# Optimization experiments

Measured on AMD Instinct MI355X. Metric: run time of the kernel, lower is better.

Reference implementation:

```python
import jax, jax.numpy as jnp
import numpy as np

B, S, D, H = 4, 4096, 1024, 8
HD = D // H  # head dims, FFT length for circular convolution


def setup_inputs() -> dict:
    key = jax.random.key(0)
    k1, k2, k3 = jax.random.split(key, 3)
    x = jax.random.normal(k1, (B, S, D), dtype=jnp.float32)
    # torch nn.Linear(D, 3D, bias=False) -> store as [D, 3D] for x @ W
    w_qkv = jax.random.normal(k2, (D, 3 * D), dtype=jnp.float32) * (1.0 / np.sqrt(D))
    w_out = jax.random.normal(k3, (D, D), dtype=jnp.float32) * (1.0 / np.sqrt(D))
    return {"x": x, "w_qkv": w_qkv, "w_out": w_out}


def reference(x, w_qkv, w_out):
    # HRR self-attention (causal, norm=False, dropout in eval mode => identity).
    b, s, d = x.shape
    qkv = x @ w_qkv                               # [B,S,3D]
    q, k, v = jnp.split(qkv, 3, axis=-1)
    q = q.reshape(b, s, H, HD)
    k = k.reshape(b, s, H, HD)
    v = v.reshape(b, s, H, HD)
    # Holographic binding: circular convolution k (*) v == ifft(fft(k)*fft(v))
    fq = jnp.fft.fft(q, axis=-1)                  # [B,S,H,HD] complex
    fk = jnp.fft.fft(k, axis=-1)
    fv = jnp.fft.fft(v, axis=-1)
    kv = fk * fv                                  # bound key-value pairs (freq domain)
    kv = jnp.cumsum(kv, axis=1)                   # causal aggregation over sequence
    # Unbinding via circular correlation with the query: ifft(S * conj(fft(q)))
    vals = jnp.fft.ifft(kv * jnp.conj(fq), axis=-1).real.astype(x.dtype)
    vals = vals.reshape(b, s, d)
    return vals @ w_out
```

## Files before the change

### kernel.cpp

```cpp
#include <hip/hip_runtime.h>

static constexpr int BB = 4;
static constexpr int SS = 4096;
static constexpr int DD = 1024;
static constexpr int HH = 8;
static constexpr int HD = 128;
static constexpr int CS = 32;
static constexpr int NCHUNK = SS / CS;
static constexpr int MROWS = BB * SS;

typedef __attribute__((ext_vector_type(8))) short bfrag;
typedef __attribute__((ext_vector_type(4))) float floatx4;

__device__ __forceinline__ float bf2f(unsigned int u) {
    return __uint_as_float((u & 0xFFFFu) << 16);
}
__device__ __forceinline__ unsigned short f2bf(float f) {
    unsigned int x = __float_as_uint(f);
    unsigned int r = x + 0x7FFFu + ((x >> 16) & 1u);
    return (unsigned short)(r >> 16);
}
__device__ __forceinline__ unsigned int pack_rne(float a, float b) {
    return ((unsigned int)f2bf(a)) | (((unsigned int)f2bf(b)) << 16);
}

__device__ __forceinline__ void async_copy16(const void* g, void* l) {
    __builtin_amdgcn_global_load_lds(
        (const __attribute__((address_space(1))) unsigned int*)g,
        (__attribute__((address_space(3))) unsigned int*)l, 16, 0, 0);
}

struct cpx { float re, im; };

__device__ __forceinline__ cpx cadd(cpx a, cpx b) { return {a.re + b.re, a.im + b.im}; }
__device__ __forceinline__ cpx csub(cpx a, cpx b) { return {a.re - b.re, a.im - b.im}; }
__device__ __forceinline__ cpx cmul(cpx a, cpx b) {
    return { fmaf(a.re, b.re, -a.im * b.im), fmaf(a.re, b.im, a.im * b.re) };
}
__device__ __forceinline__ cpx cmul_cj(cpx a, cpx b) {
    return { fmaf(a.re, b.re, a.im * b.im), fmaf(a.im, b.re, -a.re * b.im) };
}
__device__ __forceinline__ cpx shflx(cpx x, int m) {
    return { __shfl_xor(x.re, m), __shfl_xor(x.im, m) };
}
__device__ __forceinline__ cpx shfl_at(cpx x, int src) {
    return { __shfl(x.re, src), __shfl(x.im, src) };
}

__device__ __forceinline__ int pair_lane_even(int l) {
    int m = (int)(__brev((unsigned)l) >> 26);
    int mp = (64 - m) & 63;
    return (int)(__brev((unsigned)mp) >> 26);
}

__device__ __forceinline__ void make_tw(int lane, cpx tw[7]) {
    const float NEG2PI = -6.28318530717958647692f;
    float a0 = NEG2PI * (float)lane * (1.0f / 128.0f);
    tw[0] = { __cosf(a0), __sinf(a0) };
    int d = 32;
#pragma unroll
    for (int s = 1; s <= 6; ++s) {
        int i = lane & (d - 1);
        float a = NEG2PI * (float)i / (float)(2 * d);
        tw[s] = { __cosf(a), __sinf(a) };
        d >>= 1;
    }
}

__device__ __forceinline__ void fft128_fwd(cpx& x0, cpx& x1, const cpx tw[7], int lane) {
    cpx a = x0, b = x1;
    x0 = cadd(a, b);
    x1 = cmul(csub(a, b), tw[0]);
    int d = 32;
#pragma unroll
    for (int s = 1; s <= 6; ++s) {
        const bool up = (lane & d) != 0;
        cpx o0 = shflx(x0, d);
        cpx o1 = shflx(x1, d);
        cpx s0 = cadd(x0, o0);
        cpx s1 = cadd(x1, o1);
        cpx d0 = cmul(csub(o0, x0), tw[s]);
        cpx d1 = cmul(csub(o1, x1), tw[s]);
        x0 = up ? d0 : s0;
        x1 = up ? d1 : s1;
        d >>= 1;
    }
}

__device__ __forceinline__ void fft128_inv(cpx& x0, cpx& x1, const cpx tw[7], int lane) {
    int d = 1;
#pragma unroll
    for (int s = 6; s >= 1; --s) {
        const bool up = (lane & d) != 0;
        cpx o0 = shflx(x0, d);
        cpx o1 = shflx(x1, d);
        cpx b0 = up ? x0 : o0;
        cpx a0 = up ? o0 : x0;
        cpx b1 = up ? x1 : o1;
        cpx a1 = up ? o1 : x1;
        cpx t0 = cmul_cj(b0, tw[s]);
        cpx t1 = cmul_cj(b1, tw[s]);
        x0 = up ? csub(a0, t0) : cadd(a0, t0);
        x1 = up ? csub(a1, t1) : cadd(a1, t1);
        d <<= 1;
    }
    cpx t = cmul_cj(x1, tw[0]);
    cpx a = x0;
    const float inv = 0.0078125f;
    x0 = { (a.re + t.re) * inv, (a.im + t.im) * inv };
    x1 = { (a.re - t.re) * inv, (a.im - t.im) * inv };
}

__global__ __launch_bounds__(256) void convert_bf16(const float* __restrict__ X,
                                                    unsigned short* __restrict__ Y)
{
    const size_t i = ((size_t)blockIdx.x * 256 + threadIdx.x) * 8;
    float4 v0 = *reinterpret_cast<const float4*>(X + i);
    float4 v1 = *reinterpret_cast<const float4*>(X + i + 4);
    uint4 p = { pack_rne(v0.x, v0.y), pack_rne(v0.z, v0.w),
                pack_rne(v1.x, v1.y), pack_rne(v1.z, v1.w) };
    *reinterpret_cast<uint4*>(Y + i) = p;
}

__global__ __launch_bounds__(256) void transpose_rn(const float* __restrict__ W,
                                                    unsigned short* __restrict__ T,
                                                    int K, int N)
{
    __shared__ float tile[32][33];
    const int n0 = blockIdx.x * 32, k0 = blockIdx.y * 32;
    const int r = threadIdx.x >> 5, c = threadIdx.x & 31;
#pragma unroll
    for (int i = 0; i < 4; ++i)
        tile[r + 8 * i][c] = W[(size_t)(k0 + r + 8 * i) * N + n0 + c];
    __syncthreads();
#pragma unroll
    for (int i = 0; i < 4; ++i) {
        float v = tile[c][r + 8 * i];
        T[(size_t)(n0 + r + 8 * i) * K + k0 + c] = f2bf(v);
    }
}

template <typename OutT>
__global__ __launch_bounds__(256) void gemm_bt(const unsigned short* __restrict__ A,
                                               const unsigned short* __restrict__ Bt,
                                               OutT* __restrict__ C,
                                               int M, int N, int K)
{
    __shared__ __align__(16) unsigned short As[128 * 32];
    __shared__ __align__(16) unsigned short Bs[128 * 32];
    const int tid = threadIdx.x, lane = tid & 63, w = tid >> 6;
    const int wr = w >> 1, wc = w & 1;
    const int m0 = blockIdx.y * 128, n0 = blockIdx.x * 128;

    floatx4 acc[4][4];
#pragma unroll
    for (int i = 0; i < 4; ++i)
#pragma unroll
        for (int j = 0; j < 4; ++j) { floatx4 z = {0.f, 0.f, 0.f, 0.f}; acc[i][j] = z; }

    for (int kt = 0; kt < K; kt += 32) {
#pragma unroll
        for (int i = 0; i < 2; ++i) {
            const int is = 2 * w + i;
            const size_t aoff = (size_t)(m0 + 16 * is + (lane >> 2)) * K + kt + (lane & 3) * 8;
            const size_t boff = (size_t)(n0 + 16 * is + (lane >> 2)) * K + kt + (lane & 3) * 8;
            async_copy16(A + aoff, &As[512 * is]);
            async_copy16(Bt + boff, &Bs[512 * is]);
        }
        __syncthreads();

        bfrag af[4], bf_[4];
#pragma unroll
        for (int t = 0; t < 4; ++t)
            af[t] = *reinterpret_cast<const bfrag*>(
                &As[(64 * wr + 16 * t + (lane & 15)) * 32 + (lane >> 4) * 8]);
#pragma unroll
        for (int t = 0; t < 4; ++t)
            bf_[t] = *reinterpret_cast<const bfrag*>(
                &Bs[(64 * wc + 16 * t + (lane & 15)) * 32 + (lane >> 4) * 8]);
#pragma unroll
        for (int i = 0; i < 4; ++i)
#pragma unroll
            for (int j = 0; j < 4; ++j)
                acc[i][j] = __builtin_amdgcn_mfma_f32_16x16x32_bf16(af[i], bf_[j], acc[i][j], 0, 0, 0);
        __syncthreads();
    }

#pragma unroll
    for (int i = 0; i < 4; ++i)
#pragma unroll
        for (int j = 0; j < 4; ++j)
#pragma unroll
            for (int r = 0; r < 4; ++r) {
                const int row = m0 + 64 * wr + 16 * i + (lane >> 4) * 4 + r;
                const int col = n0 + 64 * wc + 16 * j + (lane & 15);
                float v = acc[i][j][r];
                if constexpr (sizeof(OutT) == 2)
                    C[(size_t)row * N + col] = (OutT)f2bf(v);
                else
                    C[(size_t)row * N + col] = (OutT)v;
            }
}

__global__ __launch_bounds__(256) void hrr_phaseA(const unsigned short* __restrict__ qkv,
                                                  unsigned int* __restrict__ P,
                                                  float* __restrict__ totals)
{
    const int blk = blockIdx.x;
    const int bh = blk / NCHUNK;
    const int chunk = blk % NCHUNK;
    const int b = bh >> 3, h = bh & 7;
    const int tid = threadIdx.x;
    const int wave = tid >> 6, lane = tid & 63;

    cpx tw[7];
    make_tw(lane, tw);
    const int pl0 = pair_lane_even(lane);
    const int pl1 = lane ^ 63;

    cpx acc0 = {0.f, 0.f}, acc1 = {0.f, 0.f};
    const int s0 = chunk * CS + wave * (CS / 4);
    for (int i = 0; i < CS / 4; ++i) {
        const int s = s0 + i;
        const unsigned short* base = qkv + (size_t)(b * SS + s) * 3072 + h * 128;
        cpx z0 = { bf2f(base[1024 + lane]),      bf2f(base[2048 + lane]) };
        cpx z1 = { bf2f(base[1024 + 64 + lane]), bf2f(base[2048 + 64 + lane]) };
        fft128_fwd(z0, z1, tw, lane);
        cpx sq0 = cmul(z0, z0);
        cpx sq1 = cmul(z1, z1);
        cpx sp0 = shfl_at(sq0, pl0);
        cpx sp1 = shfl_at(sq1, pl1);
        cpx p0 = { 0.25f * (sq0.im + sp0.im), 0.25f * (sp0.re - sq0.re) };
        cpx p1 = { 0.25f * (sq1.im + sp1.im), 0.25f * (sp1.re - sq1.re) };
        acc0 = cadd(acc0, p0);
        acc1 = cadd(acc1, p1);
        unsigned int* prow = P + ((size_t)bh * SS + s) * 128;
        prow[lane]      = pack_rne(p0.re, p0.im);
        prow[64 + lane] = pack_rne(p1.re, p1.im);
    }

    __shared__ float red[4][256];
    red[wave][lane * 2 + 0] = acc0.re;
    red[wave][lane * 2 + 1] = acc0.im;
    red[wave][128 + lane * 2 + 0] = acc1.re;
    red[wave][128 + lane * 2 + 1] = acc1.im;
    __syncthreads();

    float s4 = red[0][tid] + red[1][tid] + red[2][tid] + red[3][tid];
    totals[((size_t)bh * NCHUNK + chunk) * 256 + tid] = s4;
}

__global__ __launch_bounds__(256) void hrr_phaseB(float* __restrict__ totals)
{
    const int bh = blockIdx.x;
    const int t = threadIdx.x;
    float run = 0.f;
#pragma unroll 4
    for (int c = 0; c < NCHUNK; ++c) {
        const size_t idx = ((size_t)bh * NCHUNK + c) * 256 + t;
        float v = totals[idx];
        totals[idx] = run;
        run += v;
    }
}

__global__ __launch_bounds__(256) void hrr_phaseC(const unsigned short* __restrict__ qkv,
                                                  const unsigned int* __restrict__ P,
                                                  const float* __restrict__ totals,
                                                  unsigned short* __restrict__ vals)
{
    __shared__ float Pf[CS * 256];

    const int blk = blockIdx.x;
    const int bh = blk / NCHUNK;
    const int chunk = blk % NCHUNK;
    const int b = bh >> 3, h = bh & 7;
    const int tid = threadIdx.x;
    const int wave = tid >> 6, lane = tid & 63;

    cpx tw[7];
    make_tw(lane, tw);
    const int pl0 = pair_lane_even(lane);
    const int pl1 = lane ^ 63;

#pragma unroll
    for (int it = 0; it < CS / 4; ++it) {
        const int sl = it * 4 + wave;
        const int s = chunk * CS + sl;
        const unsigned int* prow = P + ((size_t)bh * SS + s) * 128;
        unsigned int a = prow[lane];
        unsigned int c = prow[64 + lane];
        float2 fa = { bf2f(a), bf2f(a >> 16) };
        float2 fc = { bf2f(c), bf2f(c >> 16) };
        *reinterpret_cast<float2*>(&Pf[sl * 256 + 2 * lane]) = fa;
        *reinterpret_cast<float2*>(&Pf[sl * 256 + 128 + 2 * lane]) = fc;
    }
    __syncthreads();

    {
        float run = totals[((size_t)bh * NCHUNK + chunk) * 256 + tid];
#pragma unroll 8
        for (int s = 0; s < CS; ++s) {
            run += Pf[s * 256 + tid];
            Pf[s * 256 + tid] = run;
        }
    }
    __syncthreads();

    for (int i = 0; i < CS / 8; ++i) {
        const int sl = wave * (CS / 4) + 2 * i;
        const int s1 = chunk * CS + sl;
        const unsigned short* b1 = qkv + (size_t)(b * SS + s1) * 3072 + h * 128;
        const unsigned short* b2 = b1 + 3072;
        cpx z0 = { bf2f(b1[lane]),      bf2f(b2[lane]) };
        cpx z1 = { bf2f(b1[64 + lane]), bf2f(b2[64 + lane]) };
        fft128_fwd(z0, z1, tw, lane);
        cpx B0 = shfl_at(z0, pl0);
        cpx B1 = shfl_at(z1, pl1);
        cpx cf1_0 = { 0.5f * (z0.re + B0.re), 0.5f * (B0.im - z0.im) };
        cpx cf1_1 = { 0.5f * (z1.re + B1.re), 0.5f * (B1.im - z1.im) };
        cpx cf2_0 = { 0.5f * (z0.im + B0.im), 0.5f * (z0.re - B0.re) };
        cpx cf2_1 = { 0.5f * (z1.im + B1.im), 0.5f * (z1.re - B1.re) };

        const float* r1 = &Pf[sl * 256];
        const float* r2 = r1 + 256;
        float2 t0 = *reinterpret_cast<const float2*>(&r1[2 * lane]);
        float2 t1 = *reinterpret_cast<const float2*>(&r1[128 + 2 * lane]);
        float2 t2 = *reinterpret_cast<const float2*>(&r2[2 * lane]);
        float2 t3 = *reinterpret_cast<const float2*>(&r2[128 + 2 * lane]);
        cpx C1_0 = { t0.x, t0.y }, C1_1 = { t1.x, t1.y };
        cpx C2_0 = { t2.x, t2.y }, C2_1 = { t3.x, t3.y };

        cpx a0 = cmul(C1_0, cf1_0), w0 = cmul(C2_0, cf2_0);
        cpx a1 = cmul(C1_1, cf1_1), w1 = cmul(C2_1, cf2_1);
        cpx u0 = { a0.re - w0.im, a0.im + w0.re };
        cpx u1 = { a1.re - w1.im, a1.im + w1.re };
        fft128_inv(u0, u1, tw, lane);

        unsigned short* o1 = vals + (size_t)(b * SS + s1) * DD + h * 128;
        unsigned short* o2 = o1 + DD;
        o1[lane]      = f2bf(u0.re);
        o1[64 + lane] = f2bf(u1.re);
        o2[lane]      = f2bf(u0.im);
        o2[64 + lane] = f2bf(u1.im);
    }
}

extern "C" void kernel_launch(void* const* d_in, const int* in_sizes, int n_in,
                              void* d_out, int out_size, void* d_ws, size_t ws_size,
                              hipStream_t stream) {
    const float* x     = (const float*)d_in[0];
    const float* w_qkv = (const float*)d_in[1];
    const float* w_out = (const float*)d_in[2];
    float* out = (float*)d_out;

    unsigned short* qkv  = (unsigned short*)d_ws;
    unsigned short* xb   = qkv + (size_t)MROWS * 3072;
    unsigned short* vals = xb + (size_t)MROWS * DD;
    unsigned int* P      = (unsigned int*)(vals + (size_t)MROWS * DD);
    float* totals        = (float*)(P + (size_t)32 * SS * 128);
    unsigned short* wqkvt = (unsigned short*)(totals + (size_t)32 * NCHUNK * 256);
    unsigned short* woutt = wqkvt + (size_t)3072 * 1024;

    convert_bf16<<<(MROWS * DD) / (256 * 8), 256, 0, stream>>>(x, xb);
    transpose_rn<<<dim3(3072 / 32, 1024 / 32), 256, 0, stream>>>(w_qkv, wqkvt, 1024, 3072);
    transpose_rn<<<dim3(1024 / 32, 1024 / 32), 256, 0, stream>>>(w_out, woutt, 1024, 1024);

    gemm_bt<unsigned short><<<dim3(3072 / 128, MROWS / 128), 256, 0, stream>>>(
        xb, wqkvt, qkv, MROWS, 3072, DD);

    hrr_phaseA<<<BB * HH * NCHUNK, 256, 0, stream>>>(qkv, P, totals);

    hrr_phaseB<<<BB * HH, 256, 0, stream>>>(totals);

    hrr_phaseC<<<BB * HH * NCHUNK, 256, 0, stream>>>(qkv, P, totals, vals);

    gemm_bt<float><<<dim3(DD / 128, MROWS / 128), 256, 0, stream>>>(
        vals, woutt, out, MROWS, DD, DD);
}
```

Measured before the change: 433.6 us.

## Use 32x32x16 MFMA with K=64 tiles and per-head panel QKV layout

Rewrites the GEMM to use 32x32x16 bf16 MFMA instructions with a 64-deep K tile, which halves the number of barrier-separated K iterations and gives larger fragments per LDS read. The QKV GEMM now writes its output as contiguous per-head panels of 128 columns, so the HRR phases read each head's row as one contiguous 256-byte run instead of striding by 3072. The LDS layout has no padding or swizzle, so the fragment reads may hit bank conflicts, and the panel-layout stores are scattered across planes.

```diff
diff --git a/kernel.cpp b/kernel.cpp
--- a/kernel.cpp
+++ b/kernel.cpp
@@ -10,7 +10,7 @@
 static constexpr int MROWS = BB * SS;
 
 typedef __attribute__((ext_vector_type(8))) short bfrag;
-typedef __attribute__((ext_vector_type(4))) float floatx4;
+typedef __attribute__((ext_vector_type(16))) float floatx16;
 
 __device__ __forceinline__ float bf2f(unsigned int u) {
     return __uint_as_float((u & 0xFFFFu) << 16);
@@ -140,69 +140,84 @@
     }
 }
 
-template <typename OutT>
-__global__ __launch_bounds__(256) void gemm_bt(const unsigned short* __restrict__ A,
-                                               const unsigned short* __restrict__ Bt,
-                                               OutT* __restrict__ C,
-                                               int M, int N, int K)
-{
-    __shared__ __align__(16) unsigned short As[128 * 32];
-    __shared__ __align__(16) unsigned short Bs[128 * 32];
+template <typename OutT, bool PANEL>
+__global__ __launch_bounds__(256) void gemm_bt32(const unsigned short* __restrict__ A,
+                                                 const unsigned short* __restrict__ Bt,
+                                                 OutT* __restrict__ C,
+                                                 int M, int N, int K)
+{
+    __shared__ __align__(16) unsigned short As[128 * 64];
+    __shared__ __align__(16) unsigned short Bs[128 * 64];
     const int tid = threadIdx.x, lane = tid & 63, w = tid >> 6;
     const int wr = w >> 1, wc = w & 1;
     const int m0 = blockIdx.y * 128, n0 = blockIdx.x * 128;
 
-    floatx4 acc[4][4];
-#pragma unroll
-    for (int i = 0; i < 4; ++i)
-#pragma unroll
-        for (int j = 0; j < 4; ++j) { floatx4 z = {0.f, 0.f, 0.f, 0.f}; acc[i][j] = z; }
-
-    for (int kt = 0; kt < K; kt += 32) {
-#pragma unroll
-        for (int i = 0; i < 2; ++i) {
-            const int is = 2 * w + i;
-            const size_t aoff = (size_t)(m0 + 16 * is + (lane >> 2)) * K + kt + (lane & 3) * 8;
-            const size_t boff = (size_t)(n0 + 16 * is + (lane >> 2)) * K + kt + (lane & 3) * 8;
-            async_copy16(A + aoff, &As[512 * is]);
-            async_copy16(Bt + boff, &Bs[512 * is]);
+    floatx16 acc[2][2];
+#pragma unroll
+    for (int i = 0; i < 2; ++i)
+#pragma unroll
+        for (int j = 0; j < 2; ++j)
+#pragma unroll
+            for (int r = 0; r < 16; ++r) acc[i][j][r] = 0.f;
+
+    const int srow = lane >> 3, scol = (lane & 7) * 8;
+
+    for (int kt = 0; kt < K; kt += 64) {
+#pragma unroll
+        for (int i = 0; i < 4; ++i) {
+            const int sg = 4 * w + i;
+            const size_t aoff = (size_t)(m0 + 8 * sg + srow) * K + kt + scol;
+            const size_t boff = (size_t)(n0 + 8 * sg + srow) * K + kt + scol;
+            async_copy16(A + aoff, &As[sg * 512]);
+            async_copy16(Bt + boff, &Bs[sg * 512]);
         }
         __syncthreads();
 
-        bfrag af[4], bf_[4];
-#pragma unroll
-        for (int t = 0; t < 4; ++t)
-            af[t] = *reinterpret_cast<const bfrag*>(
-                &As[(64 * wr + 16 * t + (lane & 15)) * 32 + (lane >> 4) * 8]);
-#pragma unroll
-        for (int t = 0; t < 4; ++t)
-            bf_[t] = *reinterpret_cast<const bfrag*>(
-                &Bs[(64 * wc + 16 * t + (lane & 15)) * 32 + (lane >> 4) * 8]);
-#pragma unroll
-        for (int i = 0; i < 4; ++i)
-#pragma unroll
-            for (int j = 0; j < 4; ++j)
-                acc[i][j] = __builtin_amdgcn_mfma_f32_16x16x32_bf16(af[i], bf_[j], acc[i][j], 0, 0, 0);
+        const int fr = lane & 31, fk = (lane >> 5) * 8;
+#pragma unroll
+        for (int kh = 0; kh < 64; kh += 16) {
+            bfrag af[2], bf_[2];
+#pragma unroll
+            for (int t = 0; t < 2; ++t) {
+                af[t]  = *reinterpret_cast<const bfrag*>(
+                    &As[(64 * wr + 32 * t + fr) * 64 + kh + fk]);
+                bf_[t] = *reinterpret_cast<const bfrag*>(
+                    &Bs[(64 * wc + 32 * t + fr) * 64 + kh + fk]);
+            }
+#pragma unroll
+            for (int i = 0; i < 2; ++i)
+#pragma unroll
+                for (int j = 0; j < 2; ++j)
+                    acc[i][j] = __builtin_amdgcn_mfma_f32_32x32x16_bf16(
+                        af[i], bf_[j], acc[i][j], 0, 0, 0);
+        }
         __syncthreads();
     }
 
-#pragma unroll
-    for (int i = 0; i < 4; ++i)
-#pragma unroll
-        for (int j = 0; j < 4; ++j)
-#pragma unroll
-            for (int r = 0; r < 4; ++r) {
-                const int row = m0 + 64 * wr + 16 * i + (lane >> 4) * 4 + r;
-                const int col = n0 + 64 * wc + 16 * j + (lane & 15);
+    OutT* Cb;
+    size_t rstride;
+    if constexpr (PANEL) { Cb = C + (size_t)n0 * M; rstride = 128; }
+    else                 { Cb = C + n0;             rstride = (size_t)N; }
+#pragma unroll
+    for (int i = 0; i < 2; ++i)
+#pragma unroll
+        for (int j = 0; j < 2; ++j)
+#pragma unroll
+            for (int r = 0; r < 16; ++r) {
+                const int rowL = (r & 3) + 8 * (r >> 2) + 4 * (lane >> 5);
+                const int rowg = m0 + 64 * wr + 32 * i + rowL;
+                const int c    = 64 * wc + 32 * j + (lane & 31);
                 float v = acc[i][j][r];
                 if constexpr (sizeof(OutT) == 2)
-                    C[(size_t)row * N + col] = (OutT)f2bf(v);
+                    Cb[(size_t)rowg * rstride + c] = (OutT)f2bf(v);
                 else
-                    C[(size_t)row * N + col] = (OutT)v;
+                    Cb[(size_t)rowg * rstride + c] = (OutT)v;
             }
 }
 
-__global__ __launch_bounds__(256) void hrr_phaseA(const unsigned short* __restrict__ qkv,
+static constexpr size_t PLANE = (size_t)MROWS * 128;
+
+__global__ __launch_bounds__(256) void hrr_phaseA(const unsigned short* __restrict__ qkvp,
                                                   unsigned int* __restrict__ P,
                                                   float* __restrict__ totals)
 {
@@ -218,13 +233,17 @@
     const int pl0 = pair_lane_even(lane);
     const int pl1 = lane ^ 63;
 
+    const unsigned short* kpl = qkvp + (size_t)(8 + h) * PLANE + (size_t)(b * SS) * 128;
+    const unsigned short* vpl = qkvp + (size_t)(16 + h) * PLANE + (size_t)(b * SS) * 128;
+
     cpx acc0 = {0.f, 0.f}, acc1 = {0.f, 0.f};
     const int s0 = chunk * CS + wave * (CS / 4);
     for (int i = 0; i < CS / 4; ++i) {
         const int s = s0 + i;
-        const unsigned short* base = qkv + (size_t)(b * SS + s) * 3072 + h * 128;
-        cpx z0 = { bf2f(base[1024 + lane]),      bf2f(base[2048 + lane]) };
-        cpx z1 = { bf2f(base[1024 + 64 + lane]), bf2f(base[2048 + 64 + lane]) };
+        const unsigned short* kr = kpl + (size_t)s * 128;
+        const unsigned short* vr = vpl + (size_t)s * 128;
+        cpx z0 = { bf2f(kr[lane]),      bf2f(vr[lane]) };
+        cpx z1 = { bf2f(kr[64 + lane]), bf2f(vr[64 + lane]) };
         fft128_fwd(z0, z1, tw, lane);
         cpx sq0 = cmul(z0, z0);
         cpx sq1 = cmul(z1, z1);
@@ -264,7 +283,7 @@
     }
 }
 
-__global__ __launch_bounds__(256) void hrr_phaseC(const unsigned short* __restrict__ qkv,
+__global__ __launch_bounds__(256) void hrr_phaseC(const unsigned short* __restrict__ qkvp,
                                                   const unsigned int* __restrict__ P,
                                                   const float* __restrict__ totals,
                                                   unsigned short* __restrict__ vals)
@@ -307,11 +326,13 @@
     }
     __syncthreads();
 
+    const unsigned short* qpl = qkvp + (size_t)h * PLANE + (size_t)(b * SS) * 128;
+
     for (int i = 0; i < CS / 8; ++i) {
         const int sl = wave * (CS / 4) + 2 * i;
         const int s1 = chunk * CS + sl;
-        const unsigned short* b1 = qkv + (size_t)(b * SS + s1) * 3072 + h * 128;
-        const unsigned short* b2 = b1 + 3072;
+        const unsigned short* b1 = qpl + (size_t)s1 * 128;
+        const unsigned short* b2 = b1 + 128;
         cpx z0 = { bf2f(b1[lane]),      bf2f(b2[lane]) };
         cpx z1 = { bf2f(b1[64 + lane]), bf2f(b2[64 + lane]) };
         fft128_fwd(z0, z1, tw, lane);
@@ -366,7 +387,7 @@
     transpose_rn<<<dim3(3072 / 32, 1024 / 32), 256, 0, stream>>>(w_qkv, wqkvt, 1024, 3072);
     transpose_rn<<<dim3(1024 / 32, 1024 / 32), 256, 0, stream>>>(w_out, woutt, 1024, 1024);
 
-    gemm_bt<unsigned short><<<dim3(3072 / 128, MROWS / 128), 256, 0, stream>>>(
+    gemm_bt32<unsigned short, true><<<dim3(3072 / 128, MROWS / 128), 256, 0, stream>>>(
         xb, wqkvt, qkv, MROWS, 3072, DD);
 
     hrr_phaseA<<<BB * HH * NCHUNK, 256, 0, stream>>>(qkv, P, totals);
@@ -375,6 +396,6 @@
 
     hrr_phaseC<<<BB * HH * NCHUNK, 256, 0, stream>>>(qkv, P, totals, vals);
 
-    gemm_bt<float><<<dim3(DD / 128, MROWS / 128), 256, 0, stream>>>(
+    gemm_bt32<float, false><<<dim3(DD / 128, MROWS / 128), 256, 0, stream>>>(
         vals, woutt, out, MROWS, DD, DD);
 }
```

After: 490.1 us. 1.13x slower.
